# Performance work log

Measured on AMD Instinct MI355X. Metric: run time of the kernel, lower is better.

Reference implementation:

```python
import jax, jax.numpy as jnp
import numpy as np
from jax import lax


def _instance_loss(z1, z2, t):
    # z1, z2: [B,T,C]; t: [B,T] timestamps
    B, T, C = z1.shape
    if B == 1:
        return jnp.asarray(0.0, z1.dtype)
    N = B * T
    tf = t.reshape(N)
    diff = jnp.abs(tf[:, None] - tf[None, :])          # [N,N]
    seq = jnp.repeat(jnp.arange(B), T)                 # sequence id per row
    same_seq = seq[:, None] == seq[None, :]
    diff = jnp.where(same_seq, diff + diff.max() + 0.001, diff)
    # k=B smallest diffs per row (cross-sequence temporal neighbors)
    _, idx = lax.top_k(-diff, B)                       # [N,B]
    z1f = z1.reshape(N, C)
    z2f = z2.reshape(N, C)
    pos = jnp.sum(z1f * z2f, axis=-1)[:, None]         # [N,1]
    neg1 = jnp.einsum('nc,nkc->nk', z1f, z1f[idx])     # [N,B]
    neg2 = jnp.einsum('nc,nkc->nk', z1f, z2f[idx])     # [N,B]
    logits = jnp.concatenate([pos, neg1, neg2], axis=1)
    return -jax.nn.log_softmax(logits, axis=1)[:, 0].mean()


def _temporal_loss(z1, z2):
    B, T, C = z1.shape
    if T == 1:
        return jnp.asarray(0.0, z1.dtype)
    z = jnp.concatenate([z1, z2], axis=1)              # [B,2T,C]
    n = 2 * T
    sim = jnp.einsum('bic,bjc->bij', z, z)             # [B,2T,2T]
    # tril(sim,-1)[:,:,:-1] + triu(sim,1)[:,:,1:] == drop-diagonal shift
    i = jnp.arange(n)[:, None]
    j = jnp.arange(n - 1)[None, :]
    logits = jnp.where(j < i, sim[:, :, : n - 1], sim[:, :, 1:])  # [B,2T,2T-1]
    nls = -jax.nn.log_softmax(logits, axis=-1)
    tt = jnp.arange(T)
    return (nls[:, tt, T + tt - 1].mean() + nls[:, T + tt, tt].mean()) / 2


def _max_pool2(z):
    # F.max_pool1d(kernel=2, stride=2) over time axis (floor, drops odd tail)
    B, T, C = z.shape
    T2 = T // 2
    return z[:, : 2 * T2].reshape(B, T2, 2, C).max(axis=2)


def hierarchical_contrastive_loss(z1, z2, t, alpha=0.5, temporal_unit=0):
    B = z1.shape[0]
    loss = jnp.asarray(0.0, z1.dtype)
    d = 0
    while z1.shape[1] > 1:
        if alpha != 0:
            loss = loss + alpha * _instance_loss(z1, z2, t)
        if d >= temporal_unit and (1 - alpha) != 0:
            loss = loss + (1 - alpha) * _temporal_loss(z1, z2)
        d += 1
        z1 = _max_pool2(z1)
        z2 = _max_pool2(z2)
        Tt = t.shape[1]
        if Tt % 2 != 0:
            t = t[:, :-1]
        t = t.reshape(B, -1, 2).mean(axis=2)
    if z1.shape[1] == 1:
        if alpha != 0:
            loss = loss + alpha * _instance_loss(z1, z2, t)
        d += 1
    return loss / d


def setup_inputs() -> dict:
    key = jax.random.key(0)
    k1, k2, k3 = jax.random.split(key, 3)
    B, T, C = 8, 512, 320
    z1 = jax.random.normal(k1, (B, T, C), dtype=jnp.float32)
    z2 = jax.random.normal(k2, (B, T, C), dtype=jnp.float32)
    # irregular, increasing timestamps per sequence
    t = jnp.sort(jax.random.uniform(k3, (B, T), dtype=jnp.float32) * T, axis=1)
    return {"z1": z1, "z2": z2, "t": t}


def reference(z1, z2, t):
    return hierarchical_contrastive_loss(z1, z2, t, alpha=0.5, temporal_unit=0)
```

## Files before the change

kernel.cpp:

```cpp
#include <hip/hip_runtime.h>
#include <math.h>

#define BB 8
#define CC 320
#define ZB 2618880
#define TTOT 4088
#define NROWS 8184
#define NROWS_T 16352
#define NTBLK 720
#define PTOT 88032
#define NP1 327680
#define NP2 5120

#define FT 2618880
#define FPART 2622968
#define FROW 2799032

constexpr int kT[10]       = {512,256,128,64,32,16,8,4,2,1};
constexpr int kLogT[10]    = {9,8,7,6,5,4,3,2,1,0};
constexpr int kZBoff[10]   = {0,1310720,1966080,2293760,2457600,2539520,2580480,2600960,2611200,2616320};
constexpr int kToff[10]    = {0,0,2048,3072,3584,3840,3968,4032,4064,4080};
constexpr int kRowcum[11]  = {0,4096,6144,7168,7680,7936,8064,8128,8160,8176,8184};
constexpr int kTRowcum[10] = {0,8192,12288,14336,15360,15872,16128,16256,16320,16352};
constexpr int kTblk128[10] = {0,512,640,672,680,688,696,704,712,720};
constexpr int kNt128[9]    = {8,4,2,1,1,1,1,1,1};
constexpr int kLog128[9]   = {3,2,1,0,0,0,0,0,0};
constexpr int kPoff128[9]  = {0,65536,81920,86016,87040,87552,87808,87936,88000};

typedef short v8s __attribute__((ext_vector_type(8)));
typedef float v16f __attribute__((ext_vector_type(16)));

__device__ __forceinline__ unsigned short f2bf(float x) {
    unsigned int u = __float_as_uint(x);
    u = (u + 0x7FFFu + ((u >> 16) & 1u)) >> 16;
    return (unsigned short)u;
}
__device__ __forceinline__ float bfu(unsigned short u) {
    return __uint_as_float(((unsigned int)u) << 16);
}

__global__ void pool_lvl03(const float* __restrict__ z1,
                           const float* __restrict__ z2,
                           const float* __restrict__ t,
                           unsigned short* __restrict__ zb,
                           float* __restrict__ tpool) {
    int gid = blockIdx.x * 256 + threadIdx.x;
    if (gid < NP1) {
        int c = gid % CC;
        int rest = gid / CC;
        int ch = rest & 63;
        int b = (rest >> 6) & 7;
        int which = rest >> 9;
        const float* src =
            (which ? z2 : z1) + ((size_t)(b * 512 + ch * 8)) * CC + c;
        unsigned short* dst = zb + (size_t)which * ZB;
        float v[8];
#pragma unroll
        for (int j = 0; j < 8; j++) v[j] = src[(size_t)j * CC];
#pragma unroll
        for (int j = 0; j < 8; j++)
            dst[(size_t)(b * 512 + ch * 8 + j) * CC + c] = f2bf(v[j]);
        float m1[4];
#pragma unroll
        for (int j = 0; j < 4; j++) m1[j] = fmaxf(v[2 * j], v[2 * j + 1]);
#pragma unroll
        for (int j = 0; j < 4; j++)
            dst[kZBoff[1] + (size_t)(b * 256 + ch * 4 + j) * CC + c] =
                f2bf(m1[j]);
        float m2[2] = {fmaxf(m1[0], m1[1]), fmaxf(m1[2], m1[3])};
#pragma unroll
        for (int j = 0; j < 2; j++)
            dst[kZBoff[2] + (size_t)(b * 128 + ch * 2 + j) * CC + c] =
                f2bf(m2[j]);
        dst[kZBoff[3] + (size_t)(b * 64 + ch) * CC + c] =
            f2bf(fmaxf(m2[0], m2[1]));
    } else if (gid < NP1 + TTOT) {
        int i = gid - NP1;
        int l = 1;
#pragma unroll
        for (int q = 2; q <= 9; q++) l = (i >= kToff[q]) ? q : l;
        int rem = i - kToff[l];
        int Tl = kT[l];
        int t2 = rem & (Tl - 1);
        int b = rem >> kLogT[l];
        int win = 512 / Tl;
        const float* p = t + b * 512 + t2 * win;
        float s = 0.f;
        for (int j = 0; j < win; j++) s += p[j];
        tpool[kToff[l] + rem] = s * (1.0f / win);
    }
}

__global__ void pool_lvl49(unsigned short* __restrict__ zb) {
    int gid = blockIdx.x * 256 + threadIdx.x;
    if (gid >= NP2) return;
    int c = gid % CC;
    int r2 = gid / CC;
    int b = r2 & 7;
    int which = r2 >> 3;
    unsigned short* base = zb + (size_t)which * ZB;
    const unsigned short* src = base + kZBoff[3] + (size_t)(b * 64) * CC + c;
    float a[32];
#pragma unroll
    for (int j = 0; j < 32; j++)
        a[j] = fmaxf(bfu(src[(size_t)(2 * j) * CC]),
                     bfu(src[(size_t)(2 * j + 1) * CC]));
#pragma unroll
    for (int j = 0; j < 32; j++)
        base[kZBoff[4] + (size_t)(b * 32 + j) * CC + c] = f2bf(a[j]);
#pragma unroll
    for (int j = 0; j < 16; j++) a[j] = fmaxf(a[2 * j], a[2 * j + 1]);
#pragma unroll
    for (int j = 0; j < 16; j++)
        base[kZBoff[5] + (size_t)(b * 16 + j) * CC + c] = f2bf(a[j]);
#pragma unroll
    for (int j = 0; j < 8; j++) a[j] = fmaxf(a[2 * j], a[2 * j + 1]);
#pragma unroll
    for (int j = 0; j < 8; j++)
        base[kZBoff[6] + (size_t)(b * 8 + j) * CC + c] = f2bf(a[j]);
#pragma unroll
    for (int j = 0; j < 4; j++) a[j] = fmaxf(a[2 * j], a[2 * j + 1]);
#pragma unroll
    for (int j = 0; j < 4; j++)
        base[kZBoff[7] + (size_t)(b * 4 + j) * CC + c] = f2bf(a[j]);
#pragma unroll
    for (int j = 0; j < 2; j++) a[j] = fmaxf(a[2 * j], a[2 * j + 1]);
#pragma unroll
    for (int j = 0; j < 2; j++)
        base[kZBoff[8] + (size_t)(b * 2 + j) * CC + c] = f2bf(a[j]);
    base[kZBoff[9] + (size_t)b * CC + c] = f2bf(fmaxf(a[0], a[1]));
}

__global__ void topk_inst_all(const unsigned short* __restrict__ zb,
                              const float* __restrict__ t0,
                              const float* __restrict__ tpool,
                              float* __restrict__ rowloss) {
    int wave = threadIdx.x >> 6, lane = threadIdx.x & 63;
    int row = blockIdx.x * 4 + wave;
    if (row >= NROWS) return;
    int l = 0;
#pragma unroll
    for (int q = 1; q <= 9; q++) l = (row >= kRowcum[q]) ? q : l;
    int n = row - kRowcum[l];
    int T = kT[l];
    const float* tt = l ? tpool + kToff[l] : t0;
    int seq = n >> kLogT[l];
    float tn = tt[n];

    int idx8[8];
    if (lane < 8) {
        const float* ts = tt + lane * T;
        bool own = (lane == seq);
        int lo = 0, hi = T;
        while (lo < hi) {
            int mid = (lo + hi) >> 1;
            if (ts[mid] < tn) lo = mid + 1; else hi = mid;
        }
        int il = lo - 1, ih = lo;
        float dl = (il >= 0) ? (tn - ts[il]) : 3.0e38f;
        float dh = (ih < T) ? (ts[ih] - tn) : 3.0e38f;
#pragma unroll
        for (int r = 0; r < 8; r++) {
            bool pickLo = (dl <= dh);
            float dmin = own ? 1.0e12f : (pickLo ? dl : dh);
            int midx = own ? n : (lane * T + (pickLo ? il : ih));
            unsigned long long key =
                ((unsigned long long)__float_as_uint(dmin) << 32) |
                (unsigned int)midx;
            unsigned long long o;
            o = __shfl_xor(key, 1); key = (key < o) ? key : o;
            o = __shfl_xor(key, 2); key = (key < o) ? key : o;
            o = __shfl_xor(key, 4); key = (key < o) ? key : o;
            int widx = (int)(unsigned int)(key & 0xffffffffull);
            idx8[r] = widx;
            if (!own && widx == midx) {
                if (pickLo) { il--; dl = (il >= 0) ? (tn - ts[il]) : 3.0e38f; }
                else        { ih++; dh = (ih < T)  ? (ts[ih] - tn) : 3.0e38f; }
            }
        }
    }

    const unsigned short* z1 = zb + kZBoff[l];
    const unsigned short* z2 = zb + ZB + kZBoff[l];
    const unsigned short* z1n = z1 + (size_t)n * CC;
    const unsigned short* z2n = z2 + (size_t)n * CC;
    float a[5];
#pragma unroll
    for (int j = 0; j < 5; j++) a[j] = bfu(z1n[lane + 64 * j]);
    float part[17];
    {
        float s = 0.f;
#pragma unroll
        for (int j = 0; j < 5; j++) s += a[j] * bfu(z2n[lane + 64 * j]);
        part[0] = s;
    }
#pragma unroll
    for (int k = 0; k < 8; k++) {
        int p = __shfl(idx8[k], 0);
        const unsigned short* r1 = z1 + (size_t)p * CC;
        const unsigned short* r2 = z2 + (size_t)p * CC;
        float s1 = 0.f, s2 = 0.f;
#pragma unroll
        for (int j = 0; j < 5; j++) {
            float av = a[j];
            s1 += av * bfu(r1[lane + 64 * j]);
            s2 += av * bfu(r2[lane + 64 * j]);
        }
        part[1 + k] = s1;
        part[9 + k] = s2;
    }
#pragma unroll
    for (int q = 0; q < 17; q++) {
        float v = part[q];
        for (int off = 32; off > 0; off >>= 1) v += __shfl_xor(v, off);
        part[q] = v;
    }
    if (lane == 0) {
        float m = part[0];
#pragma unroll
        for (int q = 1; q < 17; q++) m = fmaxf(m, part[q]);
        float s = 0.f;
#pragma unroll
        for (int q = 0; q < 17; q++) s += expf(part[q] - m);
        float w = 0.05f / (float)(BB * T);
        rowloss[row] = w * (m + logf(s) - part[0]);
    }
}

__global__ void __launch_bounds__(256) temporal_mfma(
        const unsigned short* __restrict__ zb, float2* __restrict__ part) {
    int bid = blockIdx.x;
    int l = 0;
#pragma unroll
    for (int q = 1; q <= 8; q++) l = (bid >= kTblk128[q]) ? q : l;
    int rem = bid - kTblk128[l];
    int Tl = kT[l], n = 2 * Tl, nt = kNt128[l], lnt = kLog128[l];
    int ct = rem & (nt - 1);
    int rt = (rem >> lnt) & (nt - 1);
    int b = rem >> (2 * lnt);
    const unsigned short* zb1 = zb + kZBoff[l] + (size_t)b * Tl * CC;
    const unsigned short* zb2 = zb + ZB + kZBoff[l] + (size_t)b * Tl * CC;
    int row0 = rt * 128, col0 = ct * 128;
    int tid = threadIdx.x;
    int w = tid >> 6, lane = tid & 63;
    __shared__ __align__(16) unsigned short As[4096];
    __shared__ __align__(16) unsigned short Bs[4096];

    v16f acc[4];
#pragma unroll
    for (int cs = 0; cs < 4; cs++)
#pragma unroll
        for (int e = 0; e < 16; e++) acc[cs][e] = 0.f;

    int sofq[2]; const unsigned short* srcA[2]; const unsigned short* srcB[2];
    bool vA[2], vB[2];
#pragma unroll
    for (int q = 0; q < 2; q++) {
        int g = q * 256 + tid;
        int r = g & 127, kbb = g >> 7;
        sofq[q] = (r >> 5) * 1024 + (kbb >> 1) * 512 + (kbb & 1) * 256 +
                  (r & 31) * 8;
        int ka = kbb * 8;
        int gr = row0 + r;
        vA[q] = gr < n;
        srcA[q] = vA[q] ? ((gr < Tl) ? zb1 + (size_t)gr * CC + ka
                                     : zb2 + (size_t)(gr - Tl) * CC + ka)
                        : zb1;
        int gc = col0 + r;
        vB[q] = gc < n;
        srcB[q] = vB[q] ? ((gc < Tl) ? zb1 + (size_t)gc * CC + ka
                                     : zb2 + (size_t)(gc - Tl) * CC + ka)
                        : zb1;
    }

    for (int kc = 0; kc < CC; kc += 32) {
#pragma unroll
        for (int q = 0; q < 2; q++) {
            uint4 av = vA[q] ? *(const uint4*)(srcA[q] + kc)
                             : make_uint4(0, 0, 0, 0);
            uint4 bv = vB[q] ? *(const uint4*)(srcB[q] + kc)
                             : make_uint4(0, 0, 0, 0);
            *(uint4*)(As + sofq[q]) = av;
            *(uint4*)(Bs + sofq[q]) = bv;
        }
        __syncthreads();
        const unsigned short* Ab = As + w * 1024;
#pragma unroll
        for (int cc = 0; cc < 2; cc++) {
            v8s af = *(const v8s*)(Ab + cc * 512 + lane * 8);
#pragma unroll
            for (int cs = 0; cs < 4; cs++) {
                v8s bf = *(const v8s*)(Bs + cs * 1024 + cc * 512 + lane * 8);
                acc[cs] = __builtin_amdgcn_mfma_f32_32x32x16_bf16(
                    af, bf, acc[cs], 0, 0, 0);
            }
        }
        __syncthreads();
    }

    int colin = lane & 31;
    int rowhalf = 4 * (lane >> 5);
#pragma unroll
    for (int r = 0; r < 16; r++) {
        int lrow = (r & 3) + 8 * (r >> 2) + rowhalf;
        int grow = row0 + w * 32 + lrow;
        float vals[4];
        float lm = -3.0e38f;
#pragma unroll
        for (int cs = 0; cs < 4; cs++) {
            int gcol = col0 + cs * 32 + colin;
            float v = acc[cs][r];
            if (gcol >= n || gcol == grow) v = -3.0e38f;
            vals[cs] = v;
            lm = fmaxf(lm, v);
        }
#pragma unroll
        for (int off = 1; off < 32; off <<= 1)
            lm = fmaxf(lm, __shfl_xor(lm, off));
        float ls = 0.f;
#pragma unroll
        for (int cs = 0; cs < 4; cs++)
            ls += (vals[cs] > -1.0e38f) ? expf(vals[cs] - lm) : 0.f;
#pragma unroll
        for (int off = 1; off < 32; off <<= 1) ls += __shfl_xor(ls, off);
        if (colin == 0 && grow < n)
            part[kPoff128[l] + ((b * n + grow) << lnt) + ct] =
                make_float2(lm, ls);
    }
}

__global__ void merge_all(const unsigned short* __restrict__ zb,
                          const float2* __restrict__ part,
                          float* __restrict__ rowloss) {
    int wave = threadIdx.x >> 6, lane = threadIdx.x & 63;
    int row = blockIdx.x * 4 + wave;
    if (row >= NROWS_T) return;
    int l = 0;
#pragma unroll
    for (int q = 1; q <= 8; q++) l = (row >= kTRowcum[q]) ? q : l;
    int r = row - kTRowcum[l];
    int Tl = kT[l], n = 2 * Tl, nt = kNt128[l], lnt = kLog128[l];
    int b = r >> (kLogT[l] + 1);
    int rr = r & (n - 1);
    float m = -3.0e38f, s = 0.f;
    if (lane < nt) {
        float2 p = part[kPoff128[l] + ((b * n + rr) << lnt) + lane];
        m = p.x; s = p.y;
    }
    float M = m;
#pragma unroll
    for (int off = 1; off < 64; off <<= 1) M = fmaxf(M, __shfl_xor(M, off));
    float e = (lane < nt) ? s * expf(m - M) : 0.f;
#pragma unroll
    for (int off = 1; off < 64; off <<= 1) e += __shfl_xor(e, off);
    int tloc = rr & (Tl - 1);
    const unsigned short* za = zb + kZBoff[l] + (size_t)(b * Tl + tloc) * CC;
    const unsigned short* zc = zb + ZB + kZBoff[l] + (size_t)(b * Tl + tloc) * CC;
    float cs = 0.f;
#pragma unroll
    for (int j = 0; j < 5; j++)
        cs += bfu(za[lane + 64 * j]) * bfu(zc[lane + 64 * j]);
#pragma unroll
    for (int off = 1; off < 64; off <<= 1) cs += __shfl_xor(cs, off);
    if (lane == 0) {
        float w = 0.025f / (float)(BB * Tl);
        rowloss[NROWS + row] = w * (M + logf(e) - cs);
    }
}

__global__ void reduce_kernel(const float* __restrict__ rowloss,
                              float* __restrict__ out) {
    __shared__ float sm[16];
    int tid = threadIdx.x;
    float s = 0.f;
    for (int i = tid; i < NROWS + NROWS_T; i += 1024) s += rowloss[i];
#pragma unroll
    for (int off = 32; off > 0; off >>= 1) s += __shfl_xor(s, off);
    if ((tid & 63) == 0) sm[tid >> 6] = s;
    __syncthreads();
    if (tid < 64) {
        float v = (tid < 16) ? sm[tid] : 0.f;
#pragma unroll
        for (int off = 8; off > 0; off >>= 1) v += __shfl_xor(v, off);
        if (tid == 0) out[0] = v;
    }
}

extern "C" void kernel_launch(void* const* d_in, const int* in_sizes, int n_in,
                              void* d_out, int out_size, void* d_ws,
                              size_t ws_size, hipStream_t stream) {
    const float* z1 = (const float*)d_in[0];
    const float* z2 = (const float*)d_in[1];
    const float* t  = (const float*)d_in[2];
    float* ws = (float*)d_ws;
    unsigned short* zb = (unsigned short*)ws;
    float* tpool = ws + FT;
    float2* part = (float2*)(ws + FPART);
    float* rowloss = ws + FROW;

    pool_lvl03<<<(NP1 + TTOT + 255) / 256, 256, 0, stream>>>(z1, z2, t, zb,
                                                             tpool);
    pool_lvl49<<<(NP2 + 255) / 256, 256, 0, stream>>>(zb);
    topk_inst_all<<<NROWS / 4, 256, 0, stream>>>(zb, t, tpool, rowloss);
    temporal_mfma<<<NTBLK, 256, 0, stream>>>(zb, part);
    merge_all<<<(NROWS_T + 3) / 4, 256, 0, stream>>>(zb, part, rowloss);
    reduce_kernel<<<1, 1024, 0, stream>>>(rowloss, (float*)d_out);
}
```

Measured before the change: 117.4 us.

## Exploit symmetry of temporal similarity matrix and extract positive logits from GEMM tiles

The temporal similarity matrix is symmetric, so the kernel now computes only upper-triangular 128x128 tiles. Off-diagonal tiles produce both row-wise and column-wise partial log-sum-exp values, and diagonal tiles reuse the A tile as B instead of loading it twice. The positive-pair logit is read out of the accumulator in the tile that holds the cross diagonal, so merge_all no longer recomputes a dot product from global memory and becomes one thread per row. The cost is an extra column-reduction pass through shared memory and a block barrier in every tile.

```diff
diff --git a/kernel.cpp b/kernel.cpp
--- a/kernel.cpp
+++ b/kernel.cpp
@@ -7,14 +7,16 @@
 #define TTOT 4088
 #define NROWS 8184
 #define NROWS_T 16352
-#define NTBLK 720
+#define NTBLK 440
 #define PTOT 88032
+#define XTOT 8176
 #define NP1 327680
 #define NP2 5120
 
 #define FT 2618880
 #define FPART 2622968
 #define FROW 2799032
+#define FCROSS 2823568
 
 constexpr int kT[10]       = {512,256,128,64,32,16,8,4,2,1};
 constexpr int kLogT[10]    = {9,8,7,6,5,4,3,2,1,0};
@@ -22,10 +24,12 @@
 constexpr int kToff[10]    = {0,0,2048,3072,3584,3840,3968,4032,4064,4080};
 constexpr int kRowcum[11]  = {0,4096,6144,7168,7680,7936,8064,8128,8160,8176,8184};
 constexpr int kTRowcum[10] = {0,8192,12288,14336,15360,15872,16128,16256,16320,16352};
-constexpr int kTblk128[10] = {0,512,640,672,680,688,696,704,712,720};
 constexpr int kNt128[9]    = {8,4,2,1,1,1,1,1,1};
 constexpr int kLog128[9]   = {3,2,1,0,0,0,0,0,0};
 constexpr int kPoff128[9]  = {0,65536,81920,86016,87040,87552,87808,87936,88000};
+constexpr int kScount[9]   = {36,10,3,1,1,1,1,1,1};
+constexpr int kSblkcum[10] = {0,288,368,392,400,408,416,424,432,440};
+constexpr int kXoff[9]     = {0,4096,6144,7168,7680,7936,8064,8128,8160};
 
 typedef short v8s __attribute__((ext_vector_type(8)));
 typedef float v16f __attribute__((ext_vector_type(16)));
@@ -228,16 +232,21 @@
 }
 
 __global__ void __launch_bounds__(256) temporal_mfma(
-        const unsigned short* __restrict__ zb, float2* __restrict__ part) {
+        const unsigned short* __restrict__ zb, float2* __restrict__ part,
+        float* __restrict__ crossbuf) {
     int bid = blockIdx.x;
     int l = 0;
 #pragma unroll
-    for (int q = 1; q <= 8; q++) l = (bid >= kTblk128[q]) ? q : l;
-    int rem = bid - kTblk128[l];
-    int Tl = kT[l], n = 2 * Tl, nt = kNt128[l], lnt = kLog128[l];
-    int ct = rem & (nt - 1);
-    int rt = (rem >> lnt) & (nt - 1);
-    int b = rem >> (2 * lnt);
+    for (int q = 1; q <= 8; q++) l = (bid >= kSblkcum[q]) ? q : l;
+    int rem = bid - kSblkcum[l];
+    int cnt = kScount[l];
+    int Tl = kT[l], n = 2 * Tl, lnt = kLog128[l];
+    int b = rem / cnt;
+    int pr = rem - b * cnt;
+    int rt = 0, width = kNt128[l];
+    while (pr >= width) { pr -= width; rt++; width--; }
+    int ct = rt + pr;
+    bool diag = (rt == ct);
     const unsigned short* zb1 = zb + kZBoff[l] + (size_t)b * Tl * CC;
     const unsigned short* zb2 = zb + ZB + kZBoff[l] + (size_t)b * Tl * CC;
     int row0 = rt * 128, col0 = ct * 128;
@@ -245,6 +254,7 @@
     int w = tid >> 6, lane = tid & 63;
     __shared__ __align__(16) unsigned short As[4096];
     __shared__ __align__(16) unsigned short Bs[4096];
+    __shared__ float2 cred[4][128];
 
     v16f acc[4];
 #pragma unroll
@@ -278,19 +288,22 @@
         for (int q = 0; q < 2; q++) {
             uint4 av = vA[q] ? *(const uint4*)(srcA[q] + kc)
                              : make_uint4(0, 0, 0, 0);
-            uint4 bv = vB[q] ? *(const uint4*)(srcB[q] + kc)
-                             : make_uint4(0, 0, 0, 0);
             *(uint4*)(As + sofq[q]) = av;
-            *(uint4*)(Bs + sofq[q]) = bv;
+            if (!diag) {
+                uint4 bv = vB[q] ? *(const uint4*)(srcB[q] + kc)
+                                 : make_uint4(0, 0, 0, 0);
+                *(uint4*)(Bs + sofq[q]) = bv;
+            }
         }
         __syncthreads();
         const unsigned short* Ab = As + w * 1024;
+        const unsigned short* Bb = diag ? As : Bs;
 #pragma unroll
         for (int cc = 0; cc < 2; cc++) {
             v8s af = *(const v8s*)(Ab + cc * 512 + lane * 8);
 #pragma unroll
             for (int cs = 0; cs < 4; cs++) {
-                v8s bf = *(const v8s*)(Bs + cs * 1024 + cc * 512 + lane * 8);
+                v8s bf = *(const v8s*)(Bb + cs * 1024 + cc * 512 + lane * 8);
                 acc[cs] = __builtin_amdgcn_mfma_f32_32x32x16_bf16(
                     af, bf, acc[cs], 0, 0, 0);
             }
@@ -300,6 +313,7 @@
 
     int colin = lane & 31;
     int rowhalf = 4 * (lane >> 5);
+
 #pragma unroll
     for (int r = 0; r < 16; r++) {
         int lrow = (r & 3) + 8 * (r >> 2) + rowhalf;
@@ -327,13 +341,59 @@
             part[kPoff128[l] + ((b * n + grow) << lnt) + ct] =
                 make_float2(lm, ls);
     }
-}
-
-__global__ void merge_all(const unsigned short* __restrict__ zb,
-                          const float2* __restrict__ part,
+
+    if (ct - rt == (Tl >> 7)) {
+#pragma unroll
+        for (int r = 0; r < 16; r++) {
+            int lrow = (r & 3) + 8 * (r >> 2) + rowhalf;
+            int grow = row0 + w * 32 + lrow;
+            if (grow < Tl) {
+                int cidx = grow + Tl - col0;
+                int cs_p = cidx >> 5, colin_p = cidx & 31;
+                float cand = 0.f;
+#pragma unroll
+                for (int cs = 0; cs < 4; cs++)
+                    cand += (cs == cs_p && colin == colin_p) ? acc[cs][r] : 0.f;
+#pragma unroll
+                for (int off = 1; off < 32; off <<= 1)
+                    cand += __shfl_xor(cand, off);
+                if (colin == 0)
+                    crossbuf[kXoff[l] + b * Tl + grow] = cand;
+            }
+        }
+    }
+
+    if (!diag) {
+#pragma unroll
+        for (int cs = 0; cs < 4; cs++) {
+            float m = acc[cs][0];
+#pragma unroll
+            for (int r = 1; r < 16; r++) m = fmaxf(m, acc[cs][r]);
+            float mo = __shfl_xor(m, 32);
+            float mm = fmaxf(m, mo);
+            float s = 0.f;
+#pragma unroll
+            for (int r = 0; r < 16; r++) s += expf(acc[cs][r] - mm);
+            s += __shfl_xor(s, 32);
+            if (lane < 32) cred[w][cs * 32 + lane] = make_float2(mm, s);
+        }
+    }
+    __syncthreads();
+    if (!diag && tid < 128) {
+        float2 a0 = cred[0][tid], a1 = cred[1][tid];
+        float2 a2 = cred[2][tid], a3 = cred[3][tid];
+        float M = fmaxf(fmaxf(a0.x, a1.x), fmaxf(a2.x, a3.x));
+        float S = a0.y * expf(a0.x - M) + a1.y * expf(a1.x - M) +
+                  a2.y * expf(a2.x - M) + a3.y * expf(a3.x - M);
+        int gcol = col0 + tid;
+        part[kPoff128[l] + ((b * n + gcol) << lnt) + rt] = make_float2(M, S);
+    }
+}
+
+__global__ void merge_all(const float2* __restrict__ part,
+                          const float* __restrict__ crossbuf,
                           float* __restrict__ rowloss) {
-    int wave = threadIdx.x >> 6, lane = threadIdx.x & 63;
-    int row = blockIdx.x * 4 + wave;
+    int row = blockIdx.x * 256 + threadIdx.x;
     if (row >= NROWS_T) return;
     int l = 0;
 #pragma unroll
@@ -342,30 +402,17 @@
     int Tl = kT[l], n = 2 * Tl, nt = kNt128[l], lnt = kLog128[l];
     int b = r >> (kLogT[l] + 1);
     int rr = r & (n - 1);
-    float m = -3.0e38f, s = 0.f;
-    if (lane < nt) {
-        float2 p = part[kPoff128[l] + ((b * n + rr) << lnt) + lane];
-        m = p.x; s = p.y;
-    }
-    float M = m;
-#pragma unroll
-    for (int off = 1; off < 64; off <<= 1) M = fmaxf(M, __shfl_xor(M, off));
-    float e = (lane < nt) ? s * expf(m - M) : 0.f;
-#pragma unroll
-    for (int off = 1; off < 64; off <<= 1) e += __shfl_xor(e, off);
-    int tloc = rr & (Tl - 1);
-    const unsigned short* za = zb + kZBoff[l] + (size_t)(b * Tl + tloc) * CC;
-    const unsigned short* zc = zb + ZB + kZBoff[l] + (size_t)(b * Tl + tloc) * CC;
-    float cs = 0.f;
-#pragma unroll
-    for (int j = 0; j < 5; j++)
-        cs += bfu(za[lane + 64 * j]) * bfu(zc[lane + 64 * j]);
-#pragma unroll
-    for (int off = 1; off < 64; off <<= 1) cs += __shfl_xor(cs, off);
-    if (lane == 0) {
-        float w = 0.025f / (float)(BB * Tl);
-        rowloss[NROWS + row] = w * (M + logf(e) - cs);
-    }
+    const float2* p = part + kPoff128[l] + ((size_t)(b * n + rr) << lnt);
+    float M = -3.0e38f, S = 0.f;
+    for (int k = 0; k < nt; k++) {
+        float2 q = p[k];
+        float nM = fmaxf(M, q.x);
+        S = S * expf(M - nM) + q.y * expf(q.x - nM);
+        M = nM;
+    }
+    float cross = crossbuf[kXoff[l] + b * Tl + (rr < Tl ? rr : rr - Tl)];
+    float w = 0.025f / (float)(BB * Tl);
+    rowloss[NROWS + row] = w * (M + logf(S) - cross);
 }
 
 __global__ void reduce_kernel(const float* __restrict__ rowloss,
@@ -397,12 +444,14 @@
     float* tpool = ws + FT;
     float2* part = (float2*)(ws + FPART);
     float* rowloss = ws + FROW;
+    float* crossbuf = ws + FCROSS;
 
     pool_lvl03<<<(NP1 + TTOT + 255) / 256, 256, 0, stream>>>(z1, z2, t, zb,
                                                              tpool);
     pool_lvl49<<<(NP2 + 255) / 256, 256, 0, stream>>>(zb);
     topk_inst_all<<<NROWS / 4, 256, 0, stream>>>(zb, t, tpool, rowloss);
-    temporal_mfma<<<NTBLK, 256, 0, stream>>>(zb, part);
-    merge_all<<<(NROWS_T + 3) / 4, 256, 0, stream>>>(zb, part, rowloss);
+    temporal_mfma<<<NTBLK, 256, 0, stream>>>(zb, part, crossbuf);
+    merge_all<<<(NROWS_T + 255) / 256, 256, 0, stream>>>(part, crossbuf,
+                                                         rowloss);
     reduce_kernel<<<1, 1024, 0, stream>>>(rowloss, (float*)d_out);
 }
```

After: 116.0 us. About the same (-1.2%).
